# Kernel tuning notes

Measured on AMD Instinct MI355X. Metric: run time of the kernel, lower is better.

The kernel has to match this reference:

```python
import jax, jax.numpy as jnp
import numpy as np

B, L, D, H, R = 2, 128, 256, 8, 4
DK = D // H  # 32
EPS = 1e-6


def setup_inputs() -> dict:
    key = jax.random.key(0)
    ks = jax.random.split(key, 12)
    q = jax.random.normal(ks[0], (B, L, D), jnp.float32)
    k = jax.random.normal(ks[1], (B, L, D), jnp.float32)
    v = jax.random.normal(ks[2], (B, L, D), jnp.float32)
    t = jnp.sort(jax.random.uniform(ks[3], (B, L), jnp.float32), axis=-1)
    omega = jax.random.uniform(ks[4], (B, L, L), jnp.float32)
    mask = jnp.triu(jnp.ones((L, L), bool), 1)  # True = masked (causal)
    xav = (2.0 / (D + D)) ** 0.5
    Wq = jax.random.normal(ks[5], (D, H * DK), jnp.float32) * xav
    Wk = jax.random.normal(ks[6], (D, H * DK), jnp.float32) * xav
    Wv = jax.random.normal(ks[7], (D, H * DK), jnp.float32) * xav
    s = jax.random.uniform(ks[8], (R,), jnp.float32) + 0.1  # ODE time-decay scales
    fc_w = jax.random.normal(ks[9], (H * DK, D), jnp.float32) * xav
    fc_b = jnp.zeros((D,), jnp.float32)
    ln_g = jnp.ones((D,), jnp.float32)
    ln_b = jnp.zeros((D,), jnp.float32)
    return {"q": q, "k": k, "v": v, "t": t, "omega": omega, "mask": mask,
            "Wq": Wq, "Wk": Wk, "Wv": Wv, "s": s,
            "fc_w": fc_w, "fc_b": fc_b, "ln_g": ln_g, "ln_b": ln_b}


def _ode_proj(x, W, phi):
    # x: (B,L,D), W: (D,H*DK), phi: (B,L,L,R) time kernel
    p = x @ W                                       # (B,L,H*DK)
    y = p[:, None, :, None, :] * phi[..., None]     # (B,L,L,R,H*DK)
    y = y.reshape(B, L, L, R, H, DK)
    return y.transpose(0, 4, 1, 2, 3, 5)            # (B,H,L,L,R,DK)


def reference(q, k, v, t, omega, mask, Wq, Wk, Wv, s, fc_w, fc_b, ln_g, ln_b):
    temp = DK ** 0.5
    residual = q
    # pre-LayerNorm on q (normalize_before=True)
    mu = q.mean(-1, keepdims=True)
    var = q.var(-1, keepdims=True)
    qn = (q - mu) / jnp.sqrt(var + EPS) * ln_g + ln_b
    # continuous-time kernel phi[b,i,j,r] = exp(-|t_i - t_j| * s_r)
    dt = jnp.abs(t[:, :, None] - t[:, None, :])     # (B,L,L)
    phi = jnp.exp(-dt[..., None] * s)               # (B,L,L,R)
    q6 = _ode_proj(qn, Wq, phi)                     # (B,H,L,L,R,DK)
    k6 = _ode_proj(k, Wk, phi)
    v6 = _ode_proj(v, Wv, phi)
    # attn = (q/temp * k * omega).sum(-1).sum(-1)
    attn = jnp.einsum('bhijrd,bhijrd,bij->bhij', q6 / temp, k6, omega)
    attn = jnp.where(mask[None, None, :, :], -1e9, attn)
    attn = jax.nn.softmax(attn, axis=-1)            # (B,H,L,L)
    vsum = v6.sum(axis=4)                           # sum over R -> (B,H,L,L,DK)
    out = jnp.einsum('bhij,bhijd->bhid', attn, vsum)  # (B,H,L,DK)
    out = out.transpose(0, 2, 1, 3).reshape(B, L, H * DK)
    out = out @ fc_w + fc_b + residual              # dropout = identity (eval)
    return (out, attn)
```

## Files before the change

kernel.cpp:

```cpp
#include <hip/hip_runtime.h>

#define B_  2
#define L_  128
#define D_  256
#define H_  8
#define R_  4
#define DK_ 32
#define BL_ (B_*L_)
#define SXP 260

__device__ __forceinline__ float wredsum64(float v) {
    #pragma unroll
    for (int m = 32; m >= 1; m >>= 1) v += __shfl_xor(v, m, 64);
    return v;
}
__device__ __forceinline__ float wredmax64(float v) {
    #pragma unroll
    for (int m = 32; m >= 1; m >>= 1) v = fmaxf(v, __shfl_xor(v, m, 64));
    return v;
}

__global__ __launch_bounds__(256) void k_proj(
    const float* __restrict__ q, const float* __restrict__ k, const float* __restrict__ v,
    const float* __restrict__ Wq, const float* __restrict__ Wk, const float* __restrict__ Wv,
    const float* __restrict__ ln_g, const float* __restrict__ ln_b,
    const float* __restrict__ fc_b,
    float* __restrict__ pv, float* __restrict__ qkpart, float* __restrict__ dout)
{
    const int blk = blockIdx.x;
    const int rowTile = blk >> 4;
    const int cg = blk & 15;
    const int rbase = rowTile * 4;
    const int tid = threadIdx.x;

    __shared__ __align__(16) float sx[3][4 * SXP];
    __shared__ __align__(16) float partF[16 * 4 * 16];
    __shared__ float spq[4][16], spk[4][16];

    {
        const int r = tid >> 6, f4c = tid & 63;
        #pragma unroll
        for (int p = 0; p < 3; ++p) {
            const float* src = (p == 0 ? q : (p == 1 ? k : v)) + (size_t)(rbase + r) * D_;
            *reinterpret_cast<float4*>(&sx[p][r * SXP + f4c * 4]) =
                reinterpret_cast<const float4*>(src)[f4c];
        }
    }

    if (tid < 64) {
        const int rr = tid >> 4, cc = tid & 15;
        const int col = cg * 16 + cc;
        const size_t off = (size_t)(rbase + rr) * D_ + col;
        dout[off] = q[off] + fc_b[col];
    }
    __syncthreads();

    {
        const int r = tid >> 6, lane = tid & 63;
        float x0 = sx[0][r * SXP + lane];
        float x1 = sx[0][r * SXP + lane + 64];
        float x2 = sx[0][r * SXP + lane + 128];
        float x3 = sx[0][r * SXP + lane + 192];
        float s1 = x0 + x1 + x2 + x3;
        float s2 = x0*x0 + x1*x1 + x2*x2 + x3*x3;
        #pragma unroll
        for (int m = 32; m >= 1; m >>= 1) {
            s1 += __shfl_xor(s1, m, 64);
            s2 += __shfl_xor(s2, m, 64);
        }
        const float mu = s1 * (1.0f / D_);
        const float rs = rsqrtf(s2 * (1.0f / D_) - mu * mu + 1e-6f);
        sx[0][r * SXP + lane      ] = (x0 - mu) * rs * ln_g[lane      ] + ln_b[lane      ];
        sx[0][r * SXP + lane +  64] = (x1 - mu) * rs * ln_g[lane +  64] + ln_b[lane +  64];
        sx[0][r * SXP + lane + 128] = (x2 - mu) * rs * ln_g[lane + 128] + ln_b[lane + 128];
        sx[0][r * SXP + lane + 192] = (x3 - mu) * rs * ln_g[lane + 192] + ln_b[lane + 192];
    }
    __syncthreads();

    const int kg  = tid >> 4;
    const int row = (tid >> 2) & 3;
    const int c4  = tid & 3;
    const int gc4 = cg * 4 + c4;
    const int kbase = kg * 16;

    #pragma unroll
    for (int m = 0; m < 3; ++m) {
        const float4* W4 = reinterpret_cast<const float4*>(m == 0 ? Wq : (m == 1 ? Wk : Wv));
        float4 a = {0, 0, 0, 0};
        #pragma unroll
        for (int kk = 0; kk < 16; ++kk) {
            const int kr = kbase + kk;
            const float x = sx[m][row * SXP + kr];
            const float4 w = W4[kr * 64 + gc4];
            a.x += x * w.x; a.y += x * w.y; a.z += x * w.z; a.w += x * w.w;
        }
        *reinterpret_cast<float4*>(&partF[(kg * 16 + row * 4 + c4) * 4]) = a;
        __syncthreads();
        if (tid < 64) {
            const int rr = tid >> 4, cc = tid & 15;
            float sum = 0.f;
            #pragma unroll
            for (int g = 0; g < 16; ++g) sum += partF[g * 64 + rr * 16 + cc];
            if      (m == 0) spq[rr][cc] = sum;
            else if (m == 1) spk[rr][cc] = sum;
            else             pv[(size_t)(rbase + rr) * D_ + cg * 16 + cc] = sum;
        }
        __syncthreads();
    }

    if (tid < 64) {
        const int rr = tid >> 4, cc = tid & 15;
        float d = spq[rr][cc] * spk[rr][cc];
        #pragma unroll
        for (int m = 8; m >= 1; m >>= 1) d += __shfl_xor(d, m, 64);
        if (cc == 0) qkpart[(size_t)(rbase + rr) * 16 + cg] = d;
    }
}

__global__ __launch_bounds__(256) void k_attn(
    const float* __restrict__ t, const float* __restrict__ omega, const float* __restrict__ s,
    const float* __restrict__ pv, const float* __restrict__ qkpart,
    const float* __restrict__ fc_w, float* __restrict__ dout)
{
    const int blk = blockIdx.x;
    const int b     = blk >> 8;
    const int itile = (blk >> 3) & 31;
    const int h     = blk & 7;
    const int ibase = itile * 4;
    const int tid = threadIdx.x;

    __shared__ __align__(16) float sQKp[L_ * 16];
    __shared__ __align__(16) float sQKh[L_];
    __shared__ __align__(16) float sOm[4 * L_];
    __shared__ __align__(16) float sPhi[4 * L_], sPsi[4 * L_];
    __shared__ __align__(16) float sAttn[4 * L_];
    __shared__ __align__(16) float partF[32 * 4 * 32];
    __shared__ float st[L_], sS[R_];
    __shared__ float sMid[4][32];

    {
        const float4* qkp4 = reinterpret_cast<const float4*>(qkpart + (size_t)b * L_ * 16);
        reinterpret_cast<float4*>(sQKp)[tid]       = qkp4[tid];
        reinterpret_cast<float4*>(sQKp)[tid + 256] = qkp4[tid + 256];
        if (tid < 128)
            reinterpret_cast<float4*>(sOm)[tid] =
                reinterpret_cast<const float4*>(omega + ((size_t)(b * L_ + ibase)) * L_)[tid];
        if (tid < 32)
            reinterpret_cast<float4*>(st)[tid] =
                reinterpret_cast<const float4*>(t + (size_t)b * L_)[tid];
        if (tid < R_) sS[tid] = s[tid];
    }
    __syncthreads();

    if (tid < 128) sQKh[tid] = sQKp[tid * 16 + 2 * h] + sQKp[tid * 16 + 2 * h + 1];
    #pragma unroll
    for (int p = 0; p < 2; ++p) {
        const int idx = tid + p * 256;
        const int wi = idx >> 7, j = idx & 127;
        const float dtv = fabsf(st[ibase + wi] - st[j]);
        float Phi = 0.f, Psi = 0.f;
        #pragma unroll
        for (int r = 0; r < R_; ++r) {
            const float e = expf(-dtv * sS[r]);
            Phi += e;
            Psi += e * e;
        }
        sPhi[idx] = Phi;
        sPsi[idx] = Psi;
    }
    __syncthreads();

    const int w = tid >> 6, lane = tid & 63;
    const int i = ibase + w;
    {
        const float invtemp = 0.17677669529663687f;
        const int j0 = lane, j1 = lane + 64;
        float l0 = (j0 <= i) ? sOm[w*L_ + j0] * sPsi[w*L_ + j0] * sQKh[j0] * invtemp : -3.0e38f;
        float l1 = (j1 <= i) ? sOm[w*L_ + j1] * sPsi[w*L_ + j1] * sQKh[j1] * invtemp : -3.0e38f;
        const float mx = wredmax64(fmaxf(l0, l1));
        const float e0 = (j0 <= i) ? expf(l0 - mx) : 0.f;
        const float e1 = (j1 <= i) ? expf(l1 - mx) : 0.f;
        const float inv = 1.0f / wredsum64(e0 + e1);
        const float a0 = e0 * inv, a1 = e1 * inv;
        sAttn[w*L_ + j0] = a0;
        sAttn[w*L_ + j1] = a1;
        const size_t ab = (size_t)BL_ * D_ + (((size_t)(b * H_ + h) * L_ + i) * L_);
        dout[ab + j0] = a0;
        dout[ab + j1] = a1;
    }
    __syncthreads();

    {
        const int jg = tid >> 3, c4 = tid & 7;
        const int gc4 = h * 8 + c4;
        const float4* pv4 = reinterpret_cast<const float4*>(pv + (size_t)b * L_ * D_);
        float4 acc[4];
        #pragma unroll
        for (int ww = 0; ww < 4; ++ww) acc[ww] = make_float4(0, 0, 0, 0);
        #pragma unroll
        for (int jj = 0; jj < 4; ++jj) {
            const int j = jg + jj * 32;
            const float4 p = pv4[j * 64 + gc4];
            #pragma unroll
            for (int ww = 0; ww < 4; ++ww) {
                const float wgt = sAttn[ww*L_ + j] * sPhi[ww*L_ + j];
                acc[ww].x += wgt * p.x; acc[ww].y += wgt * p.y;
                acc[ww].z += wgt * p.z; acc[ww].w += wgt * p.w;
            }
        }
        #pragma unroll
        for (int ww = 0; ww < 4; ++ww)
            *reinterpret_cast<float4*>(&partF[(jg * 32 + ww * 8 + c4) * 4]) = acc[ww];
    }
    __syncthreads();
    if (tid < 128) {
        const int ww = tid >> 5, cc = tid & 31;
        float sum = 0.f;
        #pragma unroll
        for (int g = 0; g < 32; ++g) sum += partF[g * 128 + ww * 32 + cc];
        sMid[ww][cc] = sum;
    }
    __syncthreads();

    {
        const float4* fw4 = reinterpret_cast<const float4*>(fc_w);
        float4 a = {0, 0, 0, 0};
        #pragma unroll
        for (int cc = 0; cc < 32; ++cc) {
            const float x = sMid[w][cc];
            const float4 wv = fw4[(h * 32 + cc) * 64 + lane];
            a.x += x * wv.x; a.y += x * wv.y; a.z += x * wv.z; a.w += x * wv.w;
        }
        float* op = dout + (size_t)(b * L_ + i) * D_ + lane * 4;
        atomicAdd(op + 0, a.x);
        atomicAdd(op + 1, a.y);
        atomicAdd(op + 2, a.z);
        atomicAdd(op + 3, a.w);
    }
}

extern "C" void kernel_launch(void* const* d_in, const int* in_sizes, int n_in,
                              void* d_out, int out_size, void* d_ws, size_t ws_size,
                              hipStream_t stream) {
    const float* q     = (const float*)d_in[0];
    const float* k     = (const float*)d_in[1];
    const float* v     = (const float*)d_in[2];
    const float* t     = (const float*)d_in[3];
    const float* omega = (const float*)d_in[4];
    const float* Wq    = (const float*)d_in[6];
    const float* Wk    = (const float*)d_in[7];
    const float* Wv    = (const float*)d_in[8];
    const float* s     = (const float*)d_in[9];
    const float* fc_w  = (const float*)d_in[10];
    const float* fc_b  = (const float*)d_in[11];
    const float* ln_g  = (const float*)d_in[12];
    const float* ln_b  = (const float*)d_in[13];

    float* ws     = (float*)d_ws;
    float* pv     = ws;
    float* qkpart = ws + 65536;
    float* out    = (float*)d_out;

    hipLaunchKernelGGL(k_proj, dim3(1024), dim3(256), 0, stream,
                       q, k, v, Wq, Wk, Wv, ln_g, ln_b, fc_b, pv, qkpart, out);
    hipLaunchKernelGGL(k_attn, dim3(512), dim3(256), 0, stream,
                       t, omega, s, pv, qkpart, fc_w, out);
}
```

Baseline: 100.6 us.

## Process all heads per attention block and drop atomic output accumulation

Each attention block now covers all eight heads for a 4-row i-tile, so the grid shrinks from 512 blocks of 256 threads to 64 blocks of 512. The fc projection is done in full inside the block, with partial sums reduced in shared memory, and the residual plus bias are written with plain stores. This replaces the per-head atomicAdds and moves the residual/bias initialization out of the projection kernel. The aim is to remove atomic traffic and the redundant per-head reloads of qkpart, omega and phi. The cost is far fewer blocks on a large GPU, which may leave most CUs idle.

```diff
diff --git a/kernel.cpp b/kernel.cpp
--- a/kernel.cpp
+++ b/kernel.cpp
@@ -8,6 +8,8 @@
 #define DK_ 32
 #define BL_ (B_*L_)
 #define SXP 260
+#define SQH 132
+#define SWP 129
 
 __device__ __forceinline__ float wredsum64(float v) {
     #pragma unroll
@@ -24,8 +26,7 @@
     const float* __restrict__ q, const float* __restrict__ k, const float* __restrict__ v,
     const float* __restrict__ Wq, const float* __restrict__ Wk, const float* __restrict__ Wv,
     const float* __restrict__ ln_g, const float* __restrict__ ln_b,
-    const float* __restrict__ fc_b,
-    float* __restrict__ pv, float* __restrict__ qkpart, float* __restrict__ dout)
+    float* __restrict__ pv, float* __restrict__ qkpart)
 {
     const int blk = blockIdx.x;
     const int rowTile = blk >> 4;
@@ -45,13 +46,6 @@
             *reinterpret_cast<float4*>(&sx[p][r * SXP + f4c * 4]) =
                 reinterpret_cast<const float4*>(src)[f4c];
         }
-    }
-
-    if (tid < 64) {
-        const int rr = tid >> 4, cc = tid & 15;
-        const int col = cg * 16 + cc;
-        const size_t off = (size_t)(rbase + rr) * D_ + col;
-        dout[off] = q[off] + fc_b[col];
     }
     __syncthreads();
 
@@ -117,31 +111,31 @@
     }
 }
 
-__global__ __launch_bounds__(256) void k_attn(
+__global__ __launch_bounds__(512) void k_attn(
     const float* __restrict__ t, const float* __restrict__ omega, const float* __restrict__ s,
     const float* __restrict__ pv, const float* __restrict__ qkpart,
-    const float* __restrict__ fc_w, float* __restrict__ dout)
+    const float* __restrict__ fc_w, const float* __restrict__ fc_b,
+    const float* __restrict__ q, float* __restrict__ dout)
 {
-    const int blk = blockIdx.x;
-    const int b     = blk >> 8;
-    const int itile = (blk >> 3) & 31;
-    const int h     = blk & 7;
+    const int blk   = blockIdx.x;
+    const int b     = blk >> 5;
+    const int itile = blk & 31;
     const int ibase = itile * 4;
     const int tid = threadIdx.x;
+    const int w = tid >> 6, lane = tid & 63;
 
     __shared__ __align__(16) float sQKp[L_ * 16];
-    __shared__ __align__(16) float sQKh[L_];
+    __shared__ __align__(16) float sQKh[H_ * SQH];
     __shared__ __align__(16) float sOm[4 * L_];
     __shared__ __align__(16) float sPhi[4 * L_], sPsi[4 * L_];
-    __shared__ __align__(16) float sAttn[4 * L_];
-    __shared__ __align__(16) float partF[32 * 4 * 32];
+    __shared__ __align__(16) float sW[H_ * 4 * SWP];
+    __shared__ __align__(16) float partF[8 * 4 * 64 * 4];
+    __shared__ __align__(16) float sMid[4 * SXP];
     __shared__ float st[L_], sS[R_];
-    __shared__ float sMid[4][32];
 
     {
         const float4* qkp4 = reinterpret_cast<const float4*>(qkpart + (size_t)b * L_ * 16);
-        reinterpret_cast<float4*>(sQKp)[tid]       = qkp4[tid];
-        reinterpret_cast<float4*>(sQKp)[tid + 256] = qkp4[tid + 256];
+        reinterpret_cast<float4*>(sQKp)[tid] = qkp4[tid];
         if (tid < 128)
             reinterpret_cast<float4*>(sOm)[tid] =
                 reinterpret_cast<const float4*>(omega + ((size_t)(b * L_ + ibase)) * L_)[tid];
@@ -152,11 +146,8 @@
     }
     __syncthreads();
 
-    if (tid < 128) sQKh[tid] = sQKp[tid * 16 + 2 * h] + sQKp[tid * 16 + 2 * h + 1];
-    #pragma unroll
-    for (int p = 0; p < 2; ++p) {
-        const int idx = tid + p * 256;
-        const int wi = idx >> 7, j = idx & 127;
+    {
+        const int wi = tid >> 7, j = tid & 127;
         const float dtv = fabsf(st[ibase + wi] - st[j]);
         float Phi = 0.f, Psi = 0.f;
         #pragma unroll
@@ -165,77 +156,113 @@
             Phi += e;
             Psi += e * e;
         }
-        sPhi[idx] = Phi;
-        sPsi[idx] = Psi;
-    }
-    __syncthreads();
-
-    const int w = tid >> 6, lane = tid & 63;
-    const int i = ibase + w;
-    {
+        sPhi[wi * L_ + j] = Phi;
+        sPsi[wi * L_ + j] = Psi;
+    }
+    #pragma unroll
+    for (int p = 0; p < 2; ++p) {
+        const int idx = tid + p * 512;
+        const int j = idx >> 3, h = idx & 7;
+        sQKh[h * SQH + j] = sQKp[j * 16 + 2 * h] + sQKp[j * 16 + 2 * h + 1];
+    }
+    __syncthreads();
+
+    {
+        const int il = w >> 1;
+        const int i  = ibase + il;
+        const int hb = (w & 1) * 4;
         const float invtemp = 0.17677669529663687f;
         const int j0 = lane, j1 = lane + 64;
-        float l0 = (j0 <= i) ? sOm[w*L_ + j0] * sPsi[w*L_ + j0] * sQKh[j0] * invtemp : -3.0e38f;
-        float l1 = (j1 <= i) ? sOm[w*L_ + j1] * sPsi[w*L_ + j1] * sQKh[j1] * invtemp : -3.0e38f;
-        const float mx = wredmax64(fmaxf(l0, l1));
-        const float e0 = (j0 <= i) ? expf(l0 - mx) : 0.f;
-        const float e1 = (j1 <= i) ? expf(l1 - mx) : 0.f;
-        const float inv = 1.0f / wredsum64(e0 + e1);
-        const float a0 = e0 * inv, a1 = e1 * inv;
-        sAttn[w*L_ + j0] = a0;
-        sAttn[w*L_ + j1] = a1;
-        const size_t ab = (size_t)BL_ * D_ + (((size_t)(b * H_ + h) * L_ + i) * L_);
-        dout[ab + j0] = a0;
-        dout[ab + j1] = a1;
-    }
-    __syncthreads();
-
-    {
-        const int jg = tid >> 3, c4 = tid & 7;
-        const int gc4 = h * 8 + c4;
+        const float c0 = sOm[il*L_ + j0] * sPsi[il*L_ + j0] * invtemp;
+        const float c1 = sOm[il*L_ + j1] * sPsi[il*L_ + j1] * invtemp;
+        const float ph0 = sPhi[il*L_ + j0], ph1 = sPhi[il*L_ + j1];
+        #pragma unroll
+        for (int hh = 0; hh < 4; ++hh) {
+            const int h = hb + hh;
+            float l0 = (j0 <= i) ? c0 * sQKh[h * SQH + j0] : -3.0e38f;
+            float l1 = (j1 <= i) ? c1 * sQKh[h * SQH + j1] : -3.0e38f;
+            const float mx = wredmax64(fmaxf(l0, l1));
+            const float e0 = (j0 <= i) ? expf(l0 - mx) : 0.f;
+            const float e1 = (j1 <= i) ? expf(l1 - mx) : 0.f;
+            const float inv = 1.0f / wredsum64(e0 + e1);
+            const float a0 = e0 * inv, a1 = e1 * inv;
+            const size_t ab = (size_t)BL_ * D_ + (((size_t)(b * H_ + h) * L_ + i) * L_);
+            dout[ab + j0] = a0;
+            dout[ab + j1] = a1;
+            sW[(h * 4 + il) * SWP + j0] = a0 * ph0;
+            sW[(h * 4 + il) * SWP + j1] = a1 * ph1;
+        }
+    }
+    __syncthreads();
+
+    {
+        const int c = lane, jg = w;
+        const int h = c >> 3;
         const float4* pv4 = reinterpret_cast<const float4*>(pv + (size_t)b * L_ * D_);
         float4 acc[4];
         #pragma unroll
-        for (int ww = 0; ww < 4; ++ww) acc[ww] = make_float4(0, 0, 0, 0);
-        #pragma unroll
-        for (int jj = 0; jj < 4; ++jj) {
-            const int j = jg + jj * 32;
-            const float4 p = pv4[j * 64 + gc4];
+        for (int il = 0; il < 4; ++il) acc[il] = make_float4(0, 0, 0, 0);
+        #pragma unroll
+        for (int jj = 0; jj < 16; ++jj) {
+            const int j = jg * 16 + jj;
+            const float4 p = pv4[j * 64 + c];
             #pragma unroll
-            for (int ww = 0; ww < 4; ++ww) {
-                const float wgt = sAttn[ww*L_ + j] * sPhi[ww*L_ + j];
-                acc[ww].x += wgt * p.x; acc[ww].y += wgt * p.y;
-                acc[ww].z += wgt * p.z; acc[ww].w += wgt * p.w;
+            for (int il = 0; il < 4; ++il) {
+                const float wgt = sW[(h * 4 + il) * SWP + j];
+                acc[il].x += wgt * p.x; acc[il].y += wgt * p.y;
+                acc[il].z += wgt * p.z; acc[il].w += wgt * p.w;
             }
         }
         #pragma unroll
-        for (int ww = 0; ww < 4; ++ww)
-            *reinterpret_cast<float4*>(&partF[(jg * 32 + ww * 8 + c4) * 4]) = acc[ww];
-    }
-    __syncthreads();
-    if (tid < 128) {
-        const int ww = tid >> 5, cc = tid & 31;
-        float sum = 0.f;
-        #pragma unroll
-        for (int g = 0; g < 32; ++g) sum += partF[g * 128 + ww * 32 + cc];
-        sMid[ww][cc] = sum;
-    }
-    __syncthreads();
-
-    {
+        for (int il = 0; il < 4; ++il)
+            *reinterpret_cast<float4*>(&partF[((jg * 4 + il) * 64 + c) * 4]) = acc[il];
+    }
+    __syncthreads();
+    if (tid < 256) {
+        const int il = tid >> 6, c = tid & 63;
+        float4 sum = make_float4(0, 0, 0, 0);
+        #pragma unroll
+        for (int g = 0; g < 8; ++g) {
+            const float4 p = *reinterpret_cast<float4*>(&partF[((g * 4 + il) * 64 + c) * 4]);
+            sum.x += p.x; sum.y += p.y; sum.z += p.z; sum.w += p.w;
+        }
+        *reinterpret_cast<float4*>(&sMid[il * SXP + c * 4]) = sum;
+    }
+    __syncthreads();
+
+    {
+        const int kseg = w, c4 = lane;
         const float4* fw4 = reinterpret_cast<const float4*>(fc_w);
-        float4 a = {0, 0, 0, 0};
-        #pragma unroll
-        for (int cc = 0; cc < 32; ++cc) {
-            const float x = sMid[w][cc];
-            const float4 wv = fw4[(h * 32 + cc) * 64 + lane];
-            a.x += x * wv.x; a.y += x * wv.y; a.z += x * wv.z; a.w += x * wv.w;
-        }
-        float* op = dout + (size_t)(b * L_ + i) * D_ + lane * 4;
-        atomicAdd(op + 0, a.x);
-        atomicAdd(op + 1, a.y);
-        atomicAdd(op + 2, a.z);
-        atomicAdd(op + 3, a.w);
+        float4 acc[4];
+        #pragma unroll
+        for (int r = 0; r < 4; ++r) acc[r] = make_float4(0, 0, 0, 0);
+        #pragma unroll
+        for (int kk = 0; kk < 32; ++kk) {
+            const int k = kseg * 32 + kk;
+            const float4 wv = fw4[k * 64 + c4];
+            #pragma unroll
+            for (int r = 0; r < 4; ++r) {
+                const float x = sMid[r * SXP + k];
+                acc[r].x += x * wv.x; acc[r].y += x * wv.y;
+                acc[r].z += x * wv.z; acc[r].w += x * wv.w;
+            }
+        }
+        #pragma unroll
+        for (int r = 0; r < 4; ++r)
+            *reinterpret_cast<float4*>(&partF[((kseg * 4 + r) * 64 + c4) * 4]) = acc[r];
+    }
+    __syncthreads();
+    if (tid < 256) {
+        const int r = tid >> 6, c4 = tid & 63;
+        const float4 bb = reinterpret_cast<const float4*>(fc_b)[c4];
+        const float4 res = reinterpret_cast<const float4*>(q)[((size_t)(b * L_ + ibase + r)) * 64 + c4];
+        float4 sum = make_float4(bb.x + res.x, bb.y + res.y, bb.z + res.z, bb.w + res.w);
+        #pragma unroll
+        for (int g = 0; g < 8; ++g) {
+            const float4 p = *reinterpret_cast<float4*>(&partF[((g * 4 + r) * 64 + c4) * 4]);
+            sum.x += p.x; sum.y += p.y; sum.z += p.z; sum.w += p.w;
+        }
+        reinterpret_cast<float4*>(dout)[((size_t)(b * L_ + ibase + r)) * 64 + c4] = sum;
     }
 }
 
@@ -262,7 +289,7 @@
     float* out    = (float*)d_out;
 
     hipLaunchKernelGGL(k_proj, dim3(1024), dim3(256), 0, stream,
-                       q, k, v, Wq, Wk, Wv, ln_g, ln_b, fc_b, pv, qkpart, out);
-    hipLaunchKernelGGL(k_attn, dim3(512), dim3(256), 0, stream,
-                       t, omega, s, pv, qkpart, fc_w, out);
-}
+                       q, k, v, Wq, Wk, Wv, ln_g, ln_b, pv, qkpart);
+    hipLaunchKernelGGL(k_attn, dim3(64), dim3(512), 0, stream,
+                       t, omega, s, pv, qkpart, fc_w, fc_b, q, out);
+}
```

Result: faster. 96.67 us (-3.9%).
